# Performance work log

Hardware: AMD Instinct MI355X
Metric: run time of the kernel (lower is better)

The kernel has to match this reference:

```python
import jax, jax.numpy as jnp
import numpy as np

NUM_HEADS = 8
NUM_GROUPS = 32
EPS = 1e-5


def setup_inputs() -> dict:
    key = jax.random.key(0)
    ks = jax.random.split(key, 5)
    B, C, H, W = 8, 512, 32, 32
    x = jax.random.normal(ks[0], (B, C, H, W), dtype=jnp.float32)
    norm_w = jnp.ones((C,), dtype=jnp.float32)
    norm_b = jnp.zeros((C,), dtype=jnp.float32)
    qkv_w = jax.random.normal(ks[1], (3 * C, C), dtype=jnp.float32) * (1.0 / np.sqrt(C))
    qkv_b = jax.random.normal(ks[2], (3 * C,), dtype=jnp.float32) * 0.02
    proj_w = jax.random.normal(ks[3], (C, C), dtype=jnp.float32) * (1.0 / np.sqrt(C))
    proj_b = jax.random.normal(ks[4], (C,), dtype=jnp.float32) * 0.02
    return {"x": x, "norm_w": norm_w, "norm_b": norm_b,
            "qkv_w": qkv_w, "qkv_b": qkv_b, "proj_w": proj_w, "proj_b": proj_b}


def _group_norm(x, w, b):
    # x: [B, C, T]; normalize over (C//G, T) per group
    B, C, T = x.shape
    xg = x.reshape(B, NUM_GROUPS, (C // NUM_GROUPS) * T)
    mean = xg.mean(axis=-1, keepdims=True)
    var = xg.var(axis=-1, keepdims=True)
    xn = ((xg - mean) * jax.lax.rsqrt(var + EPS)).reshape(B, C, T)
    return xn * w[None, :, None] + b[None, :, None]


def reference(x, norm_w, norm_b, qkv_w, qkv_b, proj_w, proj_b):
    B, C, H, W = x.shape
    T = H * W
    x3 = x.reshape(B, C, T)
    h = _group_norm(x3, norm_w, norm_b)
    # 1x1 conv == channel matmul: [B, 3C, T]
    qkv = jnp.einsum('oc,bct->bot', qkv_w, h) + qkv_b[None, :, None]
    nh = NUM_HEADS
    ch = C // nh
    qkv = qkv.reshape(B * nh, 3 * ch, T)
    q, k, v = jnp.split(qkv, 3, axis=1)  # each [B*nh, ch, T]
    scale = 1.0 / np.sqrt(np.sqrt(ch))
    w = jnp.einsum('bct,bcs->bts', q * scale, k * scale)  # [B*nh, T, T]
    w = jax.nn.softmax(w, axis=-1)
    a = jnp.einsum('bts,bcs->bct', w, v).reshape(B, C, T)
    out = jnp.einsum('oc,bct->bot', proj_w, a) + proj_b[None, :, None]
    return (x3 + out).reshape(B, C, H, W)
```

## Files before the change

### kernel.cpp

```cpp
#include <hip/hip_runtime.h>
#include <stdint.h>

typedef short v8s __attribute__((ext_vector_type(8)));
typedef float v4f __attribute__((ext_vector_type(4)));

#define MFMA(a, b, c) __builtin_amdgcn_mfma_f32_16x16x32_bf16((a), (b), (c), 0, 0, 0)

__device__ __forceinline__ short f2bf(float f) {
  union { float f; uint32_t u; } v; v.f = f;
  uint32_t r = v.u + 0x7fffu + ((v.u >> 16) & 1u);
  return (short)(r >> 16);
}

__device__ __forceinline__ uint32_t pack2(float a, float b) {
  union { float f; uint32_t u; } ua, ub; ua.f = a; ub.f = b;
  return __builtin_amdgcn_perm(ub.u, ua.u, 0x07060302u);
}

__device__ __forceinline__ void gload16(const void* g, void* l) {
  __builtin_amdgcn_global_load_lds((const __attribute__((address_space(1))) void*)g,
                                   (__attribute__((address_space(3))) void*)l,
                                   16, 0, 0);
}

__global__ __launch_bounds__(256) void prep_gn_kernel(
    const float* __restrict__ qkvw, const float* __restrict__ qkvb,
    const float* __restrict__ projw,
    short* __restrict__ Wq, short* __restrict__ Wp, float* __restrict__ bias2,
    const float* __restrict__ x, const float* __restrict__ gw,
    const float* __restrict__ gb, short* __restrict__ hT) {
  __shared__ float red[8];
  __shared__ short tile[16 * 1032];
  int tid = threadIdx.x;
  if (blockIdx.x >= 256) {
    int idx = (blockIdx.x - 256) * 256 + tid;
    if (idx < 1536 * 512) {
      int r = idx >> 9, c = idx & 511;
      int sec = r >> 9;
      int rr = r & 511;
      int nh = rr >> 6, cc = rr & 63;
      int o = nh * 192 + sec * 64 + cc;
      Wq[idx] = f2bf(qkvw[o * 512 + c]);
      if (c == 0) bias2[r] = qkvb[o];
    } else {
      int j = idx - 1536 * 512;
      if (j < 512 * 512) Wp[j] = f2bf(projw[j]);
    }
    return;
  }
  int b = blockIdx.x >> 5, g = blockIdx.x & 31;
  const float* xg = x + (b * 512 + g * 16) * 1024;
  float s = 0.f, ss = 0.f;
#pragma unroll
  for (int r = 0; r < 16; ++r) {
    float4 v = *(const float4*)(xg + r * 1024 + tid * 4);
    s += v.x + v.y + v.z + v.w;
    ss += v.x * v.x + v.y * v.y + v.z * v.z + v.w * v.w;
  }
#pragma unroll
  for (int off = 32; off > 0; off >>= 1) {
    s += __shfl_xor(s, off, 64);
    ss += __shfl_xor(ss, off, 64);
  }
  if ((tid & 63) == 0) { red[tid >> 6] = s; red[4 + (tid >> 6)] = ss; }
  __syncthreads();
  float S = red[0] + red[1] + red[2] + red[3];
  float SS = red[4] + red[5] + red[6] + red[7];
  float mean = S * (1.f / 16384.f);
  float var = SS * (1.f / 16384.f) - mean * mean;
  float inv = rsqrtf(var + 1e-5f);
#pragma unroll
  for (int r = 0; r < 16; ++r) {
    int c = g * 16 + r;
    float a = inv * gw[c];
    float bb = gb[c] - mean * a;
    float4 v = *(const float4*)(xg + r * 1024 + tid * 4);
    short* tr = tile + r * 1032 + tid * 4;
    tr[0] = f2bf(fmaf(v.x, a, bb));
    tr[1] = f2bf(fmaf(v.y, a, bb));
    tr[2] = f2bf(fmaf(v.z, a, bb));
    tr[3] = f2bf(fmaf(v.w, a, bb));
  }
  __syncthreads();
  int r = tid & 15, tq = tid >> 4;
  int c = g * 16 + r;
  short* dst = hT + b * 1024 * 512 + c;
  const short* src = tile + r * 1032;
#pragma unroll
  for (int i = 0; i < 64; ++i) {
    int t = i * 16 + tq;
    dst[t * 512] = src[t];
  }
}

__device__ __forceinline__ void gemm_k512(
    const short* __restrict__ Ag, const short* __restrict__ Bg,
    short* lA, short* lB, int wid, int lane, v4f acc[4][4]) {
  int r4 = lane >> 2, seg = lane & 3;
  int wr = (wid >> 1) * 64, wc = (wid & 1) * 64;
  int c16 = lane & 15, q8 = (lane >> 4) * 8;
  const short* ga = Ag + (wid * 16 + r4) * 512 + seg * 8;
  const short* gbp = Bg + (wid * 16 + r4) * 512 + seg * 8;
  for (int kt = 0; kt < 16; ++kt) {
    int k0 = kt * 32;
    gload16(ga + k0, lA + wid * 512);
    gload16(ga + 64 * 512 + k0, lA + (wid + 4) * 512);
    gload16(gbp + k0, lB + wid * 512);
    gload16(gbp + 64 * 512 + k0, lB + (wid + 4) * 512);
    __syncthreads();
    v8s af[4], bf[4];
#pragma unroll
    for (int i = 0; i < 4; ++i)
      af[i] = *(const v8s*)(lA + (wr + i * 16 + c16) * 32 + q8);
#pragma unroll
    for (int j = 0; j < 4; ++j)
      bf[j] = *(const v8s*)(lB + (wc + j * 16 + c16) * 32 + q8);
#pragma unroll
    for (int i = 0; i < 4; ++i)
#pragma unroll
      for (int j = 0; j < 4; ++j)
        acc[i][j] = MFMA(af[i], bf[j], acc[i][j]);
    __syncthreads();
  }
}

__global__ __launch_bounds__(256) void qkv_gemm_kernel(
    const short* __restrict__ hT, const short* __restrict__ Wq,
    const float* __restrict__ bias2,
    short* __restrict__ Qb, short* __restrict__ Kb, short* __restrict__ Vb) {
  __shared__ __align__(16) short smem[17408];
  short* lA = smem;
  short* lB = smem + 4096;
  short* vt = smem;
  int bm = blockIdx.x & 63, bo = blockIdx.x >> 6;
  int tid = threadIdx.x, wid = tid >> 6, lane = tid & 63;
  int wr = (wid >> 1) * 64, wc = (wid & 1) * 64;
  int q = lane >> 4, c16 = lane & 15;
  v4f acc[4][4];
#pragma unroll
  for (int i = 0; i < 4; ++i)
#pragma unroll
    for (int j = 0; j < 4; ++j) acc[i][j] = (v4f){0.f, 0.f, 0.f, 0.f};
  gemm_k512(hT + bm * 128 * 512, Wq + bo * 128 * 512, lA, lB, wid, lane, acc);
  float bv[4];
#pragma unroll
  for (int j = 0; j < 4; ++j) bv[j] = bias2[bo * 128 + wc + j * 16 + c16];
  if (bo < 8) {
    short* dst = (bo < 4) ? Qb : Kb;
    float sc = (bo < 4) ? 0.18033688f : 1.f;
    int obase = (bo & 3) * 128 + wc;
#pragma unroll
    for (int j = 0; j < 4; ++j) {
      int ocol = obase + j * 16 + c16;
      int nh = ocol >> 6, cc = ocol & 63;
#pragma unroll
      for (int i = 0; i < 4; ++i)
#pragma unroll
        for (int rr = 0; rr < 4; ++rr) {
          int n = bm * 128 + wr + i * 16 + q * 4 + rr;
          int b_ = n >> 10, t = n & 1023;
          float v = (acc[i][j][rr] + bv[j]) * sc;
          dst[b_ * 524288 + nh * 65536 + t * 64 + cc] = f2bf(v);
        }
    }
  } else {
#pragma unroll
    for (int j = 0; j < 4; ++j) {
      int ol = wc + j * 16 + c16;
#pragma unroll
      for (int i = 0; i < 4; ++i)
#pragma unroll
        for (int rr = 0; rr < 4; ++rr) {
          int nl = wr + i * 16 + q * 4 + rr;
          vt[ol * 136 + nl] = f2bf(acc[i][j][rr] + bv[j]);
        }
    }
    __syncthreads();
    int ol = tid >> 1, hf = tid & 1;
    int ovg = (bo - 8) * 128 + ol;
    const short* src = vt + ol * 136 + hf * 64;
    short* dstv = Vb + ovg * 8192 + bm * 128 + hf * 64;
#pragma unroll
    for (int m = 0; m < 8; ++m)
      *(v8s*)(dstv + m * 8) = *(const v8s*)(src + m * 8);
  }
}

__global__ __launch_bounds__(512, 4) void attn_kernel(
    const short* __restrict__ Qb, const short* __restrict__ Kb,
    const short* __restrict__ Vb, short* __restrict__ aT) {
  __shared__ __align__(16) short lds[35840];
  int hb = blockIdx.x >> 3, tt = blockIdx.x & 7;
  int b = hb >> 3, nh = hb & 7;
  int tid = threadIdx.x, wid = tid >> 6, lane = tid & 63;
  int chunk = wid >> 2, w4 = wid & 3;
  int q = lane >> 4, c16 = lane & 15;
  const short* Qh = Qb + hb * 65536;
  const short* Kh = Kb + hb * 65536;
  const short* Vh = Vb + nh * 64 * 8192 + b * 1024;
  int t0 = tt * 128 + w4 * 32;
  int sbase = chunk * 512;
  short* Kst = lds + chunk * 4096;
  short* Vst = lds + 8192 + chunk * 4096;
  short* pw = lds + 16384 + wid * 2432;
  v8s qf[2][2];
#pragma unroll
  for (int i = 0; i < 2; ++i)
#pragma unroll
    for (int kk = 0; kk < 2; ++kk)
      qf[i][kk] = *(const v8s*)(Qh + (t0 + i * 16 + c16) * 64 + kk * 32 + q * 8);
  v4f of[2][4];
  float lsum[2] = {0.f, 0.f};
#pragma unroll
  for (int i = 0; i < 2; ++i)
#pragma unroll
    for (int j = 0; j < 4; ++j) of[i][j] = (v4f){0.f, 0.f, 0.f, 0.f};
  int sidx0 = w4 * 128 + lane;
  int sidx1 = w4 * 128 + 64 + lane;
  int r0 = sidx0 >> 3, m0 = (sidx0 & 7) ^ (r0 & 7);
  int r1 = sidx1 >> 3, m1 = (sidx1 & 7) ^ (r1 & 7);
#pragma unroll 1
  for (int st = 0; st < 8; ++st) {
    int s0 = sbase + st * 64;
    gload16(Kh + (s0 + r0) * 64 + m0 * 8, Kst + (w4 * 128) * 8);
    gload16(Kh + (s0 + r1) * 64 + m1 * 8, Kst + (w4 * 128 + 64) * 8);
    gload16(Vh + r0 * 8192 + s0 + m0 * 8, Vst + (w4 * 128) * 8);
    gload16(Vh + r1 * 8192 + s0 + m1 * 8, Vst + (w4 * 128 + 64) * 8);
    __syncthreads();
    v8s kf[4][2];
#pragma unroll
    for (int j = 0; j < 4; ++j) {
      int row = j * 16 + c16;
#pragma unroll
      for (int kk = 0; kk < 2; ++kk) {
        int pc = (kk * 4 + q) ^ (c16 & 7);
        kf[j][kk] = *(const v8s*)(Kst + row * 64 + pc * 8);
      }
    }
#pragma unroll
    for (int j = 0; j < 4; ++j) {
      v4f s0v = (v4f){0.f, 0.f, 0.f, 0.f};
      s0v = MFMA(kf[j][0], qf[0][0], s0v);
      s0v = MFMA(kf[j][1], qf[0][1], s0v);
      v4f s1v = (v4f){0.f, 0.f, 0.f, 0.f};
      s1v = MFMA(kf[j][0], qf[1][0], s1v);
      s1v = MFMA(kf[j][1], qf[1][1], s1v);
      float p00 = __builtin_amdgcn_exp2f(s0v[0]);
      float p01 = __builtin_amdgcn_exp2f(s0v[1]);
      float p02 = __builtin_amdgcn_exp2f(s0v[2]);
      float p03 = __builtin_amdgcn_exp2f(s0v[3]);
      lsum[0] += (p00 + p01) + (p02 + p03);
      uint2 pk0;
      pk0.x = pack2(p00, p01);
      pk0.y = pack2(p02, p03);
      *(uint2*)(pw + c16 * 76 + j * 16 + q * 4) = pk0;
      float p10 = __builtin_amdgcn_exp2f(s1v[0]);
      float p11 = __builtin_amdgcn_exp2f(s1v[1]);
      float p12 = __builtin_amdgcn_exp2f(s1v[2]);
      float p13 = __builtin_amdgcn_exp2f(s1v[3]);
      lsum[1] += (p10 + p11) + (p12 + p13);
      uint2 pk1;
      pk1.x = pack2(p10, p11);
      pk1.y = pack2(p12, p13);
      *(uint2*)(pw + (16 + c16) * 76 + j * 16 + q * 4) = pk1;
    }
    v8s vf[4][2];
#pragma unroll
    for (int j = 0; j < 4; ++j) {
      int row = j * 16 + c16;
#pragma unroll
      for (int kk = 0; kk < 2; ++kk) {
        int pc = (kk * 4 + q) ^ (c16 & 7);
        vf[j][kk] = *(const v8s*)(Vst + row * 64 + pc * 8);
      }
    }
    asm volatile("s_waitcnt lgkmcnt(0)" ::: "memory");
    v8s pa[2][2];
#pragma unroll
    for (int i = 0; i < 2; ++i)
#pragma unroll
      for (int kk = 0; kk < 2; ++kk)
        pa[i][kk] = *(const v8s*)(pw + (i * 16 + c16) * 76 + kk * 32 + q * 8);
#pragma unroll
    for (int i = 0; i < 2; ++i)
#pragma unroll
      for (int j = 0; j < 4; ++j) {
        of[i][j] = MFMA(pa[i][0], vf[j][0], of[i][j]);
        of[i][j] = MFMA(pa[i][1], vf[j][1], of[i][j]);
      }
    __syncthreads();
  }
#pragma unroll
  for (int i = 0; i < 2; ++i) {
    lsum[i] += __shfl_xor(lsum[i], 16, 64);
    lsum[i] += __shfl_xor(lsum[i], 32, 64);
  }
  float* ex = (float*)(lds + 16384) + w4 * 2144;
  __syncthreads();
  if (chunk == 1) {
#pragma unroll
    for (int i = 0; i < 2; ++i) {
#pragma unroll
      for (int j = 0; j < 4; ++j)
#pragma unroll
        for (int rr = 0; rr < 4; ++rr)
          ex[(i * 16 + q * 4 + rr) * 66 + j * 16 + c16] = of[i][j][rr];
      if (q == 0) ex[2112 + i * 16 + c16] = lsum[i];
    }
  }
  __syncthreads();
  if (chunk == 0) {
    short* base = aT + b * 1024 * 512 + nh * 64;
#pragma unroll
    for (int i = 0; i < 2; ++i)
#pragma unroll
      for (int rr = 0; rr < 4; ++rr) {
        int row = i * 16 + q * 4 + rr;
        float inv = 1.f / (__shfl(lsum[i], q * 4 + rr, 64) + ex[2112 + row]);
        int t = t0 + row;
#pragma unroll
        for (int j = 0; j < 4; ++j) {
          float v = (of[i][j][rr] + ex[row * 66 + j * 16 + c16]) * inv;
          base[t * 512 + j * 16 + c16] = f2bf(v);
        }
      }
  }
}

__global__ __launch_bounds__(256) void proj_gemm_kernel(
    const short* __restrict__ Wp, const short* __restrict__ aT,
    const float* __restrict__ pbias, const float* __restrict__ x,
    float* __restrict__ out) {
  __shared__ __align__(16) short smem[8192];
  short* lA = smem;
  short* lB = smem + 4096;
  int bm = blockIdx.x & 3, bn = blockIdx.x >> 2;
  int tid = threadIdx.x, wid = tid >> 6, lane = tid & 63;
  int wr = (wid >> 1) * 64, wc = (wid & 1) * 64;
  int q = lane >> 4, c16 = lane & 15;
  v4f acc[4][4];
#pragma unroll
  for (int i = 0; i < 4; ++i)
#pragma unroll
    for (int j = 0; j < 4; ++j) acc[i][j] = (v4f){0.f, 0.f, 0.f, 0.f};
  gemm_k512(Wp + bm * 128 * 512, aT + bn * 128 * 512, lA, lB, wid, lane, acc);
  int colOff[4];
#pragma unroll
  for (int j = 0; j < 4; ++j) {
    int n = bn * 128 + wc + j * 16 + c16;
    colOff[j] = (n >> 10) * 524288 + (n & 1023);
  }
#pragma unroll
  for (int i = 0; i < 4; ++i)
#pragma unroll
    for (int rr = 0; rr < 4; ++rr) {
      int o = bm * 128 + wr + i * 16 + q * 4 + rr;
      float bs = pbias[o];
      int ro = o * 1024;
#pragma unroll
      for (int j = 0; j < 4; ++j) {
        int a = colOff[j] + ro;
        out[a] = acc[i][j][rr] + bs + x[a];
      }
    }
}

extern "C" void kernel_launch(void* const* d_in, const int* in_sizes, int n_in,
                              void* d_out, int out_size, void* d_ws, size_t ws_size,
                              hipStream_t stream) {
  const float* x = (const float*)d_in[0];
  const float* nw = (const float*)d_in[1];
  const float* nb = (const float*)d_in[2];
  const float* qkvw = (const float*)d_in[3];
  const float* qkvb = (const float*)d_in[4];
  const float* projw = (const float*)d_in[5];
  const float* projb = (const float*)d_in[6];
  float* out = (float*)d_out;
  char* w = (char*)d_ws;
  short* hT = (short*)(w);
  short* aT = (short*)(w + 8388608);
  short* Qb = (short*)(w + 16777216);
  short* Kb = (short*)(w + 25165824);
  short* Vb = (short*)(w + 33554432);
  short* Wq2 = (short*)(w + 41943040);
  short* Wp2 = (short*)(w + 43515904);
  float* b2 = (float*)(w + 44040192);

  hipLaunchKernelGGL(prep_gn_kernel, dim3(4352), dim3(256), 0, stream,
                     qkvw, qkvb, projw, Wq2, Wp2, b2, x, nw, nb, hT);
  hipLaunchKernelGGL(qkv_gemm_kernel, dim3(768), dim3(256), 0, stream,
                     hT, Wq2, b2, Qb, Kb, Vb);
  hipLaunchKernelGGL(attn_kernel, dim3(512), dim3(512), 0, stream, Qb, Kb, Vb, aT);
  hipLaunchKernelGGL(proj_gemm_kernel, dim3(256), dim3(256), 0, stream,
                     Wp2, aT, projb, x, out);
}
```

Baseline: 163.1 us.

## Double GEMM K-tile to 64 with XOR-swizzled LDS layout

The shared K=512 GEMM helper now stages 64-wide K tiles instead of 32, halving the number of barrier-separated iterations. LDS rows are stored with an XOR swizzle on 16-byte chunks to avoid bank conflicts on the fragment reads, and the read offsets are adjusted to match. LDS use per block doubles for the projection GEMM, which may reduce occupancy.

```diff
diff --git a/kernel.cpp b/kernel.cpp
--- a/kernel.cpp
+++ b/kernel.cpp
@@ -93,33 +93,44 @@
   }
 }
 
-__device__ __forceinline__ void gemm_k512(
+__device__ __forceinline__ void gemm_k512_b64(
     const short* __restrict__ Ag, const short* __restrict__ Bg,
     short* lA, short* lB, int wid, int lane, v4f acc[4][4]) {
-  int r4 = lane >> 2, seg = lane & 3;
   int wr = (wid >> 1) * 64, wc = (wid & 1) * 64;
-  int c16 = lane & 15, q8 = (lane >> 4) * 8;
-  const short* ga = Ag + (wid * 16 + r4) * 512 + seg * 8;
-  const short* gbp = Bg + (wid * 16 + r4) * 512 + seg * 8;
-  for (int kt = 0; kt < 16; ++kt) {
-    int k0 = kt * 32;
-    gload16(ga + k0, lA + wid * 512);
-    gload16(ga + 64 * 512 + k0, lA + (wid + 4) * 512);
-    gload16(gbp + k0, lB + wid * 512);
-    gload16(gbp + 64 * 512 + k0, lB + (wid + 4) * 512);
+  int c16 = lane & 15, q = lane >> 4;
+  int srow = lane >> 3;
+  int sw = ((lane & 7) ^ srow) * 8;
+  const short* gaw = Ag + (wid * 32 + srow) * 512 + sw;
+  const short* gbw = Bg + (wid * 32 + srow) * 512 + sw;
+  short* lAw = lA + wid * 2048;
+  short* lBw = lB + wid * 2048;
+  int pc0 = (q ^ (c16 & 7)) * 8;
+  int pc1 = ((4 + q) ^ (c16 & 7)) * 8;
+  for (int kt = 0; kt < 8; ++kt) {
+    int k0 = kt * 64;
+#pragma unroll
+    for (int t = 0; t < 4; ++t)
+      gload16(gaw + t * 8 * 512 + k0, lAw + t * 512);
+#pragma unroll
+    for (int t = 0; t < 4; ++t)
+      gload16(gbw + t * 8 * 512 + k0, lBw + t * 512);
     __syncthreads();
-    v8s af[4], bf[4];
-#pragma unroll
-    for (int i = 0; i < 4; ++i)
-      af[i] = *(const v8s*)(lA + (wr + i * 16 + c16) * 32 + q8);
-#pragma unroll
-    for (int j = 0; j < 4; ++j)
-      bf[j] = *(const v8s*)(lB + (wc + j * 16 + c16) * 32 + q8);
-#pragma unroll
-    for (int i = 0; i < 4; ++i)
+#pragma unroll
+    for (int ks = 0; ks < 2; ++ks) {
+      int pc = ks ? pc1 : pc0;
+      v8s af[4], bf[4];
+#pragma unroll
+      for (int i = 0; i < 4; ++i)
+        af[i] = *(const v8s*)(lA + (wr + i * 16 + c16) * 64 + pc);
 #pragma unroll
       for (int j = 0; j < 4; ++j)
-        acc[i][j] = MFMA(af[i], bf[j], acc[i][j]);
+        bf[j] = *(const v8s*)(lB + (wc + j * 16 + c16) * 64 + pc);
+#pragma unroll
+      for (int i = 0; i < 4; ++i)
+#pragma unroll
+        for (int j = 0; j < 4; ++j)
+          acc[i][j] = MFMA(af[i], bf[j], acc[i][j]);
+    }
     __syncthreads();
   }
 }
@@ -130,7 +141,7 @@
     short* __restrict__ Qb, short* __restrict__ Kb, short* __restrict__ Vb) {
   __shared__ __align__(16) short smem[17408];
   short* lA = smem;
-  short* lB = smem + 4096;
+  short* lB = smem + 8192;
   short* vt = smem;
   int bm = blockIdx.x & 63, bo = blockIdx.x >> 6;
   int tid = threadIdx.x, wid = tid >> 6, lane = tid & 63;
@@ -141,7 +152,7 @@
   for (int i = 0; i < 4; ++i)
 #pragma unroll
     for (int j = 0; j < 4; ++j) acc[i][j] = (v4f){0.f, 0.f, 0.f, 0.f};
-  gemm_k512(hT + bm * 128 * 512, Wq + bo * 128 * 512, lA, lB, wid, lane, acc);
+  gemm_k512_b64(hT + bm * 128 * 512, Wq + bo * 128 * 512, lA, lB, wid, lane, acc);
   float bv[4];
 #pragma unroll
   for (int j = 0; j < 4; ++j) bv[j] = bias2[bo * 128 + wc + j * 16 + c16];
@@ -331,9 +342,9 @@
     const short* __restrict__ Wp, const short* __restrict__ aT,
     const float* __restrict__ pbias, const float* __restrict__ x,
     float* __restrict__ out) {
-  __shared__ __align__(16) short smem[8192];
+  __shared__ __align__(16) short smem[16384];
   short* lA = smem;
-  short* lB = smem + 4096;
+  short* lB = smem + 8192;
   int bm = blockIdx.x & 3, bn = blockIdx.x >> 2;
   int tid = threadIdx.x, wid = tid >> 6, lane = tid & 63;
   int wr = (wid >> 1) * 64, wc = (wid & 1) * 64;
@@ -343,7 +354,7 @@
   for (int i = 0; i < 4; ++i)
 #pragma unroll
     for (int j = 0; j < 4; ++j) acc[i][j] = (v4f){0.f, 0.f, 0.f, 0.f};
-  gemm_k512(Wp + bm * 128 * 512, aT + bn * 128 * 512, lA, lB, wid, lane, acc);
+  gemm_k512_b64(Wp + bm * 128 * 512, aT + bn * 128 * 512, lA, lB, wid, lane, acc);
   int colOff[4];
 #pragma unroll
   for (int j = 0; j < 4; ++j) {
```

Measured after the change: 160.1 us. No clear change (-1.8%).
